# Performance work log

Hardware: AMD Instinct MI355X
Metric: run time of the kernel (lower is better)

Reference implementation:

```python
import jax, jax.numpy as jnp
import numpy as np

N_P, N_W, F_IN = 512, 3584, 256
H1, O1 = 8, 32
H2, O2 = 8, 256
BATCH = 1024
NEG_SLOPE = 0.2


def _xavier(key, shape):
    fan_in, fan_out = shape[-2], shape[-1]
    lim = jnp.sqrt(6.0 / (fan_in + fan_out))
    return jax.random.uniform(key, shape, jnp.float32, -lim, lim)


def setup_inputs() -> dict:
    key = jax.random.key(0)
    ks = jax.random.split(key, 16)
    return {
        "input": jax.random.uniform(ks[0], (BATCH, N_W), jnp.float32),
        "pern_feature": jax.random.normal(ks[1], (N_P, F_IN), jnp.float32),
        "word_feature": jax.random.normal(ks[2], (N_W, F_IN), jnp.float32),
        "w1": _xavier(ks[3], (H1, F_IN, O1)),
        "a_src1": _xavier(ks[4], (H1, O1, 1)),
        "a_dst1": _xavier(ks[5], (H1, O1, 1)),
        "b1": jnp.zeros((O1,), jnp.float32),
        "w2": _xavier(ks[6], (H2, F_IN, O2)),
        "a_src2": _xavier(ks[7], (H2, F_IN, 1)),
        "a_dst2": _xavier(ks[8], (H2, F_IN, 1)),
        "b2": jnp.zeros((O2,), jnp.float32),
        "W_fc": _xavier(ks[9], (O2, 5)),
        "b_fc": jnp.zeros((5,), jnp.float32),
        "pern_adj": jax.random.randint(ks[10], (N_P, N_P), 0, 2, jnp.int32),
        "word_pern_adj": jax.random.randint(ks[11], (N_P + N_W, N_P + N_W), 0, 2, jnp.int32),
    }


def gat(h, adj, w, a_src, a_dst, bias):
    # h: [N, f_in], adj: [N, N] int, w: [H, f_in, f_out]
    h_prime = jnp.einsum('nf,hfo->hno', h, w)          # [H, N, O]
    t = jnp.tanh(h_prime)
    s_src = jnp.einsum('hno,hoi->hn', t, a_src)        # [H, N]
    s_dst = jnp.einsum('hno,hoi->hn', t, a_dst)        # [H, N]
    attn = s_src[:, :, None] + s_dst[:, None, :]       # [H, N, N]
    attn = jnp.where(attn >= 0, attn, NEG_SLOPE * attn)  # leaky_relu
    attn = jnp.where(adj[None, :, :] > 0, attn, -jnp.inf)
    attn = jax.nn.softmax(attn, axis=-1)
    out = jnp.einsum('hnm,hmo->hno', attn, h_prime)    # [H, N, O]
    return out + bias


def reference(input, pern_feature, word_feature, w1, a_src1, a_dst1, b1,
              w2, a_src2, a_dst2, b2, W_fc, b_fc, pern_adj, word_pern_adj):
    n_p = pern_feature.shape[0]
    # GAT 1 over personality graph
    h1 = gat(pern_feature, pern_adj, w1, a_src1, a_dst1, b1)       # [H1, n_p, O1]
    hiddn_pp = jnp.transpose(h1, (1, 0, 2)).reshape(n_p, -1)        # [n_p, H1*O1]
    hiddn_pp = jax.nn.elu(hiddn_pp)
    # dropout is identity in eval mode
    hiddn_wp = jnp.concatenate([word_feature, hiddn_pp], axis=0)    # [N, 256]
    h2 = gat(hiddn_wp, word_pern_adj, w2, a_src2, a_dst2, b2)       # [H2, N, O2]
    hiddn_wp2 = h2.mean(axis=0)                                     # [N, O2]
    hiddn_w = hiddn_wp2[:word_feature.shape[0], :]                  # [n_w, O2]
    x = (input @ hiddn_w) / input.sum(axis=1, keepdims=True)        # [B, O2]
    return x @ W_fc + b_fc                                          # [B, 5]
```

## Files before the change

### kernel.cpp

```cpp
#include <hip/hip_runtime.h>
#include <hip/hip_bf16.h>
#include <math.h>

#define NP 512
#define NW 3584
#define NT 4096
#define FIN 256
#define H1 8
#define O1 32
#define H2 8
#define O2 256
#define NEG 0.2f

typedef __attribute__((ext_vector_type(8))) short bf16x8;
typedef __attribute__((ext_vector_type(4))) float f32x4;

__device__ __forceinline__ unsigned short f2bf(float f) {
    unsigned u = __float_as_uint(f);
    unsigned r = (u + 0x7FFF + ((u >> 16) & 1)) >> 16;
    return (unsigned short)r;
}

__global__ void k_conv_word(const float* __restrict__ wf, unsigned short* __restrict__ abf) {
    int i = blockIdx.x * 256 + threadIdx.x;
    if (i < NW * FIN) abf[i] = f2bf(wf[i]);
}

__global__ __launch_bounds__(256) void k_gat1_hp(
    const float* __restrict__ pf, const float* __restrict__ w1,
    const float* __restrict__ a_src1, const float* __restrict__ a_dst1,
    float* __restrict__ hp1, float* __restrict__ ss1, float* __restrict__ sd1)
{
    __shared__ float feat[8][FIN];
    int t = threadIdx.x;
    int n0 = blockIdx.x * 8;
    for (int q = 0; q < 8; q++) {
        int idx = q * 256 + t;
        feat[idx >> 8][idx & 255] = pf[(n0 + (idx >> 8)) * FIN + (idx & 255)];
    }
    __syncthreads();
    int h = t >> 5, o = t & 31;
    float acc[8] = {0,0,0,0,0,0,0,0};
    const float* wcol = w1 + h * FIN * O1 + o;
    for (int f = 0; f < FIN; f++) {
        float w = wcol[f * O1];
        #pragma unroll
        for (int i = 0; i < 8; i++) acc[i] += feat[i][f] * w;
    }
    float as = a_src1[h * O1 + o];
    float ad = a_dst1[h * O1 + o];
    #pragma unroll
    for (int i = 0; i < 8; i++) {
        hp1[(n0 + i) * 256 + t] = acc[i];
        float th = tanhf(acc[i]);
        float vs = th * as, vd = th * ad;
        #pragma unroll
        for (int off = 1; off < 32; off <<= 1) {
            vs += __shfl_xor(vs, off);
            vd += __shfl_xor(vd, off);
        }
        if (o == 0) { ss1[h * NP + n0 + i] = vs; sd1[h * NP + n0 + i] = vd; }
    }
}

__global__ __launch_bounds__(256) void k_gat1_attn(
    const int* __restrict__ adj, const float* __restrict__ hp1,
    const float* __restrict__ ss1, const float* __restrict__ sd1,
    const float* __restrict__ b1, unsigned short* __restrict__ abf)
{
    __shared__ float p[2][H1][NP];
    __shared__ float den[2][H1];
    int t = threadIdx.x;
    int n0 = blockIdx.x * 2;
    for (int rr = 0; rr < 32; rr++) {
        int idx = rr * 256 + t;
        int i = idx >> 12, h = (idx >> 9) & 7, m = idx & 511;
        float a = adj[(n0 + i) * NP + m] > 0 ? 1.0f : 0.0f;
        float e = ss1[h * NP + n0 + i] + sd1[h * NP + m];
        e = fmaxf(e, NEG * e);
        p[i][h][m] = a * __expf(e);
    }
    __syncthreads();
    int w = t >> 6, l = t & 63;
    {
        int i = w & 1;
        #pragma unroll
        for (int hh = 0; hh < 4; hh++) {
            int h = (w >> 1) * 4 + hh;
            float s = 0;
            #pragma unroll
            for (int q = 0; q < 8; q++) s += p[i][h][l + 64 * q];
            #pragma unroll
            for (int off = 1; off < 64; off <<= 1) s += __shfl_xor(s, off);
            if (l == 0) den[i][h] = s;
        }
    }
    __syncthreads();
    int h = t >> 5, o = t & 31;
    float acc[2] = {0, 0};
    #pragma unroll 4
    for (int m = 0; m < NP; m++) {
        float v = hp1[m * 256 + t];
        acc[0] += p[0][h][m] * v;
        acc[1] += p[1][h][m] * v;
    }
    float bo = b1[o];
    #pragma unroll
    for (int i = 0; i < 2; i++) {
        float r = acc[i] / den[i][h] + bo;
        r = r > 0.f ? r : expm1f(r);
        abf[(NW + n0 + i) * FIN + t] = f2bf(r);
    }
}

__global__ void k_conv_w2(const float* __restrict__ w2, unsigned short* __restrict__ btbf) {
    int idx = blockIdx.x * 256 + threadIdx.x;
    int f = idx & 255, o = (idx >> 8) & 255, h = idx >> 16;
    btbf[idx] = f2bf(w2[(h * FIN + f) * O2 + o]);
}

__global__ __launch_bounds__(256) void k_pack_adj(const int* __restrict__ adj,
                                                  unsigned long long* __restrict__ packed) {
    int w = threadIdx.x >> 6, l = threadIdx.x & 63;
    int r = blockIdx.x * 4 + w;
    const int* row = adj + (size_t)r * NT;
    unsigned long long myword = 0;
    for (int chunk = 0; chunk < 64; chunk++) {
        unsigned long long mask = __ballot(row[chunk * 64 + l] != 0);
        if (l == chunk) myword = mask;
    }
    packed[r * 64 + l] = myword;
}

__global__ __launch_bounds__(256) void k_gemm_hp2(
    const unsigned short* __restrict__ abf, const unsigned short* __restrict__ btbf,
    const float* __restrict__ a_src2, const float* __restrict__ a_dst2,
    const float* __restrict__ W_fc, float* __restrict__ gpart)
{
    int bid = blockIdx.x;
    int h = bid >> 6;
    int rem = bid & 63;
    int mt = rem >> 1, nt = rem & 1;
    int w = threadIdx.x >> 6, l = threadIdx.x & 63;
    int m0 = mt * 128 + (w >> 1) * 64;
    int n0 = nt * 128 + (w & 1) * 64;
    int lr = l & 15, lq = l >> 4;
    const unsigned short* bbase = btbf + h * O2 * FIN;
    f32x4 acc[4][4];
    #pragma unroll
    for (int i = 0; i < 4; i++)
        #pragma unroll
        for (int j = 0; j < 4; j++) acc[i][j] = (f32x4){0.f, 0.f, 0.f, 0.f};
    for (int k = 0; k < FIN; k += 32) {
        bf16x8 a[4], b[4];
        int kc = k + lq * 8;
        #pragma unroll
        for (int i = 0; i < 4; i++)
            a[i] = *(const bf16x8*)(abf + (m0 + i * 16 + lr) * FIN + kc);
        #pragma unroll
        for (int j = 0; j < 4; j++)
            b[j] = *(const bf16x8*)(bbase + (n0 + j * 16 + lr) * FIN + kc);
        #pragma unroll
        for (int i = 0; i < 4; i++)
            #pragma unroll
            for (int j = 0; j < 4; j++)
                acc[i][j] = __builtin_amdgcn_mfma_f32_16x16x32_bf16(a[i], b[j], acc[i][j], 0, 0, 0);
    }
    int slice = nt * 2 + (w & 1);
    float as[4], ad[4], wfc[4][5];
    #pragma unroll
    for (int j = 0; j < 4; j++) {
        int col = n0 + j * 16 + lr;
        as[j] = a_src2[h * O2 + col];
        ad[j] = a_dst2[h * O2 + col];
        #pragma unroll
        for (int jj = 0; jj < 5; jj++) wfc[j][jj] = W_fc[col * 5 + jj];
    }
    float* base = gpart + ((size_t)h * 4 + slice) * NT * 8;
    #pragma unroll
    for (int i = 0; i < 4; i++) {
        #pragma unroll
        for (int r = 0; r < 4; r++) {
            float s[7] = {0,0,0,0,0,0,0};
            #pragma unroll
            for (int j = 0; j < 4; j++) {
                float x = acc[i][j][r];
                float th = tanhf(x);
                s[0] += th * as[j];
                s[1] += th * ad[j];
                #pragma unroll
                for (int jj = 0; jj < 5; jj++) s[2 + jj] += x * wfc[j][jj];
            }
            #pragma unroll
            for (int off = 1; off < 16; off <<= 1)
                #pragma unroll
                for (int q = 0; q < 7; q++) s[q] += __shfl_xor(s[q], off);
            if (lr == 0) {
                int m = m0 + i * 16 + lq * 4 + r;
                float* dst = base + (size_t)m * 8;
                #pragma unroll
                for (int q = 0; q < 7; q++) dst[q] = s[q];
            }
        }
    }
}

__global__ __launch_bounds__(256) void k_comb_hp2(
    const float* __restrict__ gpart,
    float* __restrict__ ss2, float* __restrict__ sd2, float* __restrict__ G)
{
    int idx = blockIdx.x * 256 + threadIdx.x;
    int h = idx >> 12, m = idx & (NT - 1);
    float s[7] = {0,0,0,0,0,0,0};
    #pragma unroll
    for (int sl = 0; sl < 4; sl++) {
        const float* p = gpart + (((size_t)h * 4 + sl) * NT + m) * 8;
        #pragma unroll
        for (int q = 0; q < 7; q++) s[q] += p[q];
    }
    ss2[h * NT + m] = s[0];
    sd2[h * NT + m] = s[1];
    #pragma unroll
    for (int j = 0; j < 5; j++) G[(h * 5 + j) * NT + m] = s[2 + j];
}

__global__ void k_cvec(const float* __restrict__ b2, const float* __restrict__ W_fc,
                       float* __restrict__ c) {
    int t = threadIdx.x;
    float v[5];
    #pragma unroll
    for (int j = 0; j < 5; j++) v[j] = b2[t] * W_fc[t * 5 + j];
    #pragma unroll
    for (int off = 1; off < 64; off <<= 1)
        #pragma unroll
        for (int j = 0; j < 5; j++) v[j] += __shfl_xor(v[j], off);
    __shared__ float red[4][5];
    int w = t >> 6, l = t & 63;
    if (l == 0) { for (int j = 0; j < 5; j++) red[w][j] = v[j]; }
    __syncthreads();
    if (t == 0)
        for (int j = 0; j < 5; j++) c[j] = red[0][j] + red[1][j] + red[2][j] + red[3][j];
}

__global__ __launch_bounds__(512) void k_gat2_attn(
    const unsigned long long* __restrict__ packed, const float* __restrict__ ss2,
    const float* __restrict__ sd2, const float* __restrict__ G,
    float* __restrict__ part)
{
    int t = threadIdx.x;
    int h = t >> 6, l = t & 63;
    int nb = blockIdx.x & 511;
    int c;
    { int b = blockIdx.x; c = b / 448; nb = b - c * 448; }
    int n0 = nb * 8;
    float ss[8];
    #pragma unroll
    for (int i = 0; i < 8; i++) ss[i] = ss2[h * NT + n0 + i];
    const float* sdh = sd2 + h * NT;
    const float* g0 = G + (h * 5 + 0) * NT;
    const float* g1 = G + (h * 5 + 1) * NT;
    const float* g2 = G + (h * 5 + 2) * NT;
    const float* g3 = G + (h * 5 + 3) * NT;
    const float* g4 = G + (h * 5 + 4) * NT;
    float den[8] = {0,0,0,0,0,0,0,0};
    float num[8][5] = {{0}};
    int mbase = c * 1024;
    int cbase = mbase >> 6;
    for (int q = 0; q < 16; q++) {
        int m = mbase + q * 64 + l;
        float sd = sdh[m];
        float ga = g0[m], gb = g1[m], gc = g2[m], gd = g3[m], ge = g4[m];
        #pragma unroll
        for (int i = 0; i < 8; i++) {
            unsigned long long word = packed[(size_t)(n0 + i) * 64 + cbase + q];
            float e = ss[i] + sd;
            e = fmaxf(e, NEG * e);
            float t0 = __expf(e);
            float pp = ((word >> l) & 1ull) ? t0 : 0.0f;
            den[i] += pp;
            num[i][0] += pp * ga;
            num[i][1] += pp * gb;
            num[i][2] += pp * gc;
            num[i][3] += pp * gd;
            num[i][4] += pp * ge;
        }
    }
    float* base = part + ((size_t)(c * 448 + nb) * 64 + h * 8) * 6;
    #pragma unroll
    for (int i = 0; i < 8; i++) {
        #pragma unroll
        for (int off = 1; off < 64; off <<= 1) {
            den[i] += __shfl_xor(den[i], off);
            #pragma unroll
            for (int j = 0; j < 5; j++) num[i][j] += __shfl_xor(num[i][j], off);
        }
        if (l == 0) {
            float* dst = base + i * 6;
            dst[0] = den[i];
            #pragma unroll
            for (int j = 0; j < 5; j++) dst[1 + j] = num[i][j];
        }
    }
}

__global__ __launch_bounds__(256) void k_gat2_comb(const float* __restrict__ part,
                                                   float* __restrict__ hf) {
    int idx = blockIdx.x * 256 + threadIdx.x;
    int n = idx >> 3, h = idx & 7;
    int nb = n >> 3, i = n & 7;
    float den = 0, num[5] = {0,0,0,0,0};
    #pragma unroll
    for (int cc = 0; cc < 4; cc++) {
        const float* p = part + ((size_t)(cc * 448 + nb) * 64 + h * 8 + i) * 6;
        den += p[0];
        #pragma unroll
        for (int j = 0; j < 5; j++) num[j] += p[1 + j];
    }
    float inv = 1.0f / (den * 8.0f);
    float v[5];
    #pragma unroll
    for (int j = 0; j < 5; j++) v[j] = num[j] * inv;
    #pragma unroll
    for (int off = 1; off < 8; off <<= 1)
        #pragma unroll
        for (int j = 0; j < 5; j++) v[j] += __shfl_xor(v[j], off);
    if (h == 0) {
        #pragma unroll
        for (int j = 0; j < 5; j++) hf[n * 5 + j] = v[j];
    }
}

__global__ __launch_bounds__(256) void k_final(
    const float* __restrict__ input, const float* __restrict__ hf,
    const float* __restrict__ cvec, const float* __restrict__ b_fc,
    float* __restrict__ out)
{
    int b = blockIdx.x, t = threadIdx.x;
    const float* row = input + (size_t)b * NW;
    float s = 0.f, a[5] = {0.f, 0.f, 0.f, 0.f, 0.f};
    for (int n = t; n < NW; n += 256) {
        float x = row[n];
        s += x;
        #pragma unroll
        for (int j = 0; j < 5; j++) a[j] += x * hf[n * 5 + j];
    }
    #pragma unroll
    for (int off = 1; off < 64; off <<= 1) {
        s += __shfl_xor(s, off);
        #pragma unroll
        for (int j = 0; j < 5; j++) a[j] += __shfl_xor(a[j], off);
    }
    __shared__ float red[4][6];
    int w = t >> 6, l = t & 63;
    if (l == 0) { red[w][0] = s; for (int j = 0; j < 5; j++) red[w][j + 1] = a[j]; }
    __syncthreads();
    if (t < 5) {
        float st = red[0][0] + red[1][0] + red[2][0] + red[3][0];
        float aj = red[0][t + 1] + red[1][t + 1] + red[2][t + 1] + red[3][t + 1];
        out[b * 5 + t] = aj / st + cvec[t] + b_fc[t];
    }
}

extern "C" void kernel_launch(void* const* d_in, const int* in_sizes, int n_in,
                              void* d_out, int out_size, void* d_ws, size_t ws_size,
                              hipStream_t stream) {
    const float* input   = (const float*)d_in[0];
    const float* pf      = (const float*)d_in[1];
    const float* wf      = (const float*)d_in[2];
    const float* w1      = (const float*)d_in[3];
    const float* a_src1  = (const float*)d_in[4];
    const float* a_dst1  = (const float*)d_in[5];
    const float* b1      = (const float*)d_in[6];
    const float* w2      = (const float*)d_in[7];
    const float* a_src2  = (const float*)d_in[8];
    const float* a_dst2  = (const float*)d_in[9];
    const float* b2      = (const float*)d_in[10];
    const float* W_fc    = (const float*)d_in[11];
    const float* b_fc    = (const float*)d_in[12];
    const int* pern_adj  = (const int*)d_in[13];
    const int* wp_adj    = (const int*)d_in[14];
    float* out = (float*)d_out;

    char* ws = (char*)d_ws;
    unsigned short* abf    = (unsigned short*)(ws);
    unsigned short* btbf   = (unsigned short*)(ws + 2097152);
    float*          hp1    = (float*)(ws + 3145728);
    float*          ss1    = (float*)(ws + 3670016);
    float*          sd1    = (float*)(ws + 3686400);
    float*          ss2    = (float*)(ws + 3702784);
    float*          sd2    = (float*)(ws + 3833856);
    float*          G      = (float*)(ws + 3964928);
    float*          hf     = (float*)(ws + 4620288);
    float*          cvec   = (float*)(ws + 4691968);
    unsigned long long* packed = (unsigned long long*)(ws + 4692480);
    float*          gpart  = (float*)(ws + 6527488);
    float*          part   = (float*)(ws + 10721792);

    k_conv_word<<<3584, 256, 0, stream>>>(wf, abf);
    k_gat1_hp<<<64, 256, 0, stream>>>(pf, w1, a_src1, a_dst1, hp1, ss1, sd1);
    k_gat1_attn<<<256, 256, 0, stream>>>(pern_adj, hp1, ss1, sd1, b1, abf);
    k_conv_w2<<<2048, 256, 0, stream>>>(w2, btbf);
    k_pack_adj<<<896, 256, 0, stream>>>(wp_adj, packed);
    k_gemm_hp2<<<512, 256, 0, stream>>>(abf, btbf, a_src2, a_dst2, W_fc, gpart);
    k_comb_hp2<<<128, 256, 0, stream>>>(gpart, ss2, sd2, G);
    k_cvec<<<1, 256, 0, stream>>>(b2, W_fc, cvec);
    k_gat2_attn<<<1792, 512, 0, stream>>>(packed, ss2, sd2, G, part);
    k_gat2_comb<<<112, 256, 0, stream>>>(part, hf);
    k_final<<<1024, 256, 0, stream>>>(input, hf, cvec, b_fc, out);
}
```

Measured before the change: 297.1 us.

## Factor attention exponentials, vectorize adjacency packing and final reduction, fast tanh

The GAT2 attention kernel now splits exp(leaky_relu(ss+sd)) into a product of precomputed exponentials, exp(ss)*exp(sd) or exp(0.2ss)*exp(0.2sd), picked by the sign of ss+sd. This removes the per-pair exp and uses an inline v_cndmask with the packed adjacency word as the mask. Per-node tables are interleaved into 8-float records for vector loads, and each block handles 16 rows with 4 heads. Adjacency packing switches to int4 loads combined by shuffles, tanh becomes an exp-based approximation, and the final kernel uses float4 loads. The factored exponentials can overflow for large scores, and register pressure rises with the 16-row accumulators.

```diff
diff --git a/kernel.cpp b/kernel.cpp
--- a/kernel.cpp
+++ b/kernel.cpp
@@ -14,11 +14,17 @@
 
 typedef __attribute__((ext_vector_type(8))) short bf16x8;
 typedef __attribute__((ext_vector_type(4))) float f32x4;
+typedef unsigned long long u64;
 
 __device__ __forceinline__ unsigned short f2bf(float f) {
     unsigned u = __float_as_uint(f);
     unsigned r = (u + 0x7FFF + ((u >> 16) & 1)) >> 16;
     return (unsigned short)r;
+}
+
+__device__ __forceinline__ float fast_tanh(float x) {
+    float ex = __expf(2.0f * x);
+    return 1.0f - 2.0f / (ex + 1.0f);
 }
 
 __global__ void k_conv_word(const float* __restrict__ wf, unsigned short* __restrict__ abf) {
@@ -120,16 +126,21 @@
 }
 
 __global__ __launch_bounds__(256) void k_pack_adj(const int* __restrict__ adj,
-                                                  unsigned long long* __restrict__ packed) {
+                                                  u64* __restrict__ packed) {
     int w = threadIdx.x >> 6, l = threadIdx.x & 63;
     int r = blockIdx.x * 4 + w;
-    const int* row = adj + (size_t)r * NT;
-    unsigned long long myword = 0;
-    for (int chunk = 0; chunk < 64; chunk++) {
-        unsigned long long mask = __ballot(row[chunk * 64 + l] != 0);
-        if (l == chunk) myword = mask;
-    }
-    packed[r * 64 + l] = myword;
+    const int4* row = (const int4*)(adj + (size_t)r * NT);
+    for (int c4 = 0; c4 < 16; c4++) {
+        int4 x = row[c4 * 64 + l];
+        u64 nib = (u64)((x.x != 0 ? 1 : 0) | (x.y != 0 ? 2 : 0) |
+                        (x.z != 0 ? 4 : 0) | (x.w != 0 ? 8 : 0));
+        u64 v = nib << (4 * (l & 15));
+        v |= __shfl_xor(v, 1);
+        v |= __shfl_xor(v, 2);
+        v |= __shfl_xor(v, 4);
+        v |= __shfl_xor(v, 8);
+        if ((l & 15) == 0) packed[(size_t)r * 64 + c4 * 4 + (l >> 4)] = v;
+    }
 }
 
 __global__ __launch_bounds__(256) void k_gemm_hp2(
@@ -185,7 +196,7 @@
             #pragma unroll
             for (int j = 0; j < 4; j++) {
                 float x = acc[i][j][r];
-                float th = tanhf(x);
+                float th = fast_tanh(x);
                 s[0] += th * as[j];
                 s[1] += th * ad[j];
                 #pragma unroll
@@ -207,7 +218,8 @@
 
 __global__ __launch_bounds__(256) void k_comb_hp2(
     const float* __restrict__ gpart,
-    float* __restrict__ ss2, float* __restrict__ sd2, float* __restrict__ G)
+    float* __restrict__ negss, float* __restrict__ Etab, float* __restrict__ Eptab,
+    float* __restrict__ T)
 {
     int idx = blockIdx.x * 256 + threadIdx.x;
     int h = idx >> 12, m = idx & (NT - 1);
@@ -218,10 +230,13 @@
         #pragma unroll
         for (int q = 0; q < 7; q++) s[q] += p[q];
     }
-    ss2[h * NT + m] = s[0];
-    sd2[h * NT + m] = s[1];
-    #pragma unroll
-    for (int j = 0; j < 5; j++) G[(h * 5 + j) * NT + m] = s[2 + j];
+    negss[idx] = -s[0];
+    Etab[idx]  = __expf(s[0]);
+    Eptab[idx] = __expf(NEG * s[0]);
+    float4 t0 = {s[1], __expf(s[1]), __expf(NEG * s[1]), s[2]};
+    float4 t1 = {s[3], s[4], s[5], s[6]};
+    *(float4*)(T + (size_t)idx * 8)     = t0;
+    *(float4*)(T + (size_t)idx * 8 + 4) = t1;
 }
 
 __global__ void k_cvec(const float* __restrict__ b2, const float* __restrict__ W_fc,
@@ -242,63 +257,72 @@
         for (int j = 0; j < 5; j++) c[j] = red[0][j] + red[1][j] + red[2][j] + red[3][j];
 }
 
-__global__ __launch_bounds__(512) void k_gat2_attn(
-    const unsigned long long* __restrict__ packed, const float* __restrict__ ss2,
-    const float* __restrict__ sd2, const float* __restrict__ G,
-    float* __restrict__ part)
+__global__ __launch_bounds__(256) void k_gat2_attn(
+    const u64* __restrict__ packed, const float* __restrict__ negss,
+    const float* __restrict__ Etab, const float* __restrict__ Eptab,
+    const float* __restrict__ T, float* __restrict__ part)
 {
     int t = threadIdx.x;
-    int h = t >> 6, l = t & 63;
-    int nb = blockIdx.x & 511;
-    int c;
-    { int b = blockIdx.x; c = b / 448; nb = b - c * 448; }
-    int n0 = nb * 8;
-    float ss[8];
-    #pragma unroll
-    for (int i = 0; i < 8; i++) ss[i] = ss2[h * NT + n0 + i];
-    const float* sdh = sd2 + h * NT;
-    const float* g0 = G + (h * 5 + 0) * NT;
-    const float* g1 = G + (h * 5 + 1) * NT;
-    const float* g2 = G + (h * 5 + 2) * NT;
-    const float* g3 = G + (h * 5 + 3) * NT;
-    const float* g4 = G + (h * 5 + 4) * NT;
-    float den[8] = {0,0,0,0,0,0,0,0};
-    float num[8][5] = {{0}};
-    int mbase = c * 1024;
-    int cbase = mbase >> 6;
+    int l = t & 63;
+    int b = blockIdx.x;
+    int hg = b & 1, c = (b >> 1) & 3, nb = b >> 3;
+    int h = hg * 4 + (t >> 6);
+    int n0 = nb * 16;
+    float ns[16], E[16], Ep[16];
+    #pragma unroll
+    for (int i = 0; i < 16; i++) {
+        ns[i] = negss[h * NT + n0 + i];
+        E[i]  = Etab[h * NT + n0 + i];
+        Ep[i] = Eptab[h * NT + n0 + i];
+    }
+    float den[16];
+    float num[16][5];
+    #pragma unroll
+    for (int i = 0; i < 16; i++) {
+        den[i] = 0.f;
+        #pragma unroll
+        for (int j = 0; j < 5; j++) num[i][j] = 0.f;
+    }
+    const float* Th = T + (size_t)h * NT * 8;
+    const u64* prow = packed + c * 16;
     for (int q = 0; q < 16; q++) {
-        int m = mbase + q * 64 + l;
-        float sd = sdh[m];
-        float ga = g0[m], gb = g1[m], gc = g2[m], gd = g3[m], ge = g4[m];
-        #pragma unroll
-        for (int i = 0; i < 8; i++) {
-            unsigned long long word = packed[(size_t)(n0 + i) * 64 + cbase + q];
-            float e = ss[i] + sd;
-            e = fmaxf(e, NEG * e);
-            float t0 = __expf(e);
-            float pp = ((word >> l) & 1ull) ? t0 : 0.0f;
+        int m = c * 1024 + q * 64 + l;
+        const float* tp = Th + (size_t)m * 8;
+        float4 t0 = *(const float4*)tp;
+        float4 t1 = *(const float4*)(tp + 4);
+        float sd = t0.x, F = t0.y, Fp = t0.z;
+        float g0 = t0.w, g1 = t1.x, g2 = t1.y, g3 = t1.z, g4 = t1.w;
+        #pragma unroll
+        for (int i = 0; i < 16; i++) {
+            u64 word = prow[(size_t)(n0 + i) * 64 + q];
+            bool sel = sd >= ns[i];
+            float f = sel ? F : Fp;
+            float e = sel ? E[i] : Ep[i];
+            float pp0 = f * e;
+            float pp;
+            asm("v_cndmask_b32 %0, 0, %1, %2" : "=v"(pp) : "v"(pp0), "s"(word));
             den[i] += pp;
-            num[i][0] += pp * ga;
-            num[i][1] += pp * gb;
-            num[i][2] += pp * gc;
-            num[i][3] += pp * gd;
-            num[i][4] += pp * ge;
+            num[i][0] = fmaf(pp, g0, num[i][0]);
+            num[i][1] = fmaf(pp, g1, num[i][1]);
+            num[i][2] = fmaf(pp, g2, num[i][2]);
+            num[i][3] = fmaf(pp, g3, num[i][3]);
+            num[i][4] = fmaf(pp, g4, num[i][4]);
         }
     }
-    float* base = part + ((size_t)(c * 448 + nb) * 64 + h * 8) * 6;
-    #pragma unroll
-    for (int i = 0; i < 8; i++) {
-        #pragma unroll
-        for (int off = 1; off < 64; off <<= 1) {
-            den[i] += __shfl_xor(den[i], off);
-            #pragma unroll
-            for (int j = 0; j < 5; j++) num[i][j] += __shfl_xor(num[i][j], off);
-        }
+    #pragma unroll
+    for (int i = 0; i < 16; i++) {
+        float v[6];
+        v[0] = den[i];
+        #pragma unroll
+        for (int j = 0; j < 5; j++) v[1 + j] = num[i][j];
+        #pragma unroll
+        for (int off = 1; off < 64; off <<= 1)
+            #pragma unroll
+            for (int k = 0; k < 6; k++) v[k] += __shfl_xor(v[k], off);
         if (l == 0) {
-            float* dst = base + i * 6;
-            dst[0] = den[i];
-            #pragma unroll
-            for (int j = 0; j < 5; j++) dst[1 + j] = num[i][j];
+            float* dst = part + (((size_t)c * NW + n0 + i) * 8 + h) * 6;
+            #pragma unroll
+            for (int k = 0; k < 6; k++) dst[k] = v[k];
         }
     }
 }
@@ -307,11 +331,10 @@
                                                    float* __restrict__ hf) {
     int idx = blockIdx.x * 256 + threadIdx.x;
     int n = idx >> 3, h = idx & 7;
-    int nb = n >> 3, i = n & 7;
     float den = 0, num[5] = {0,0,0,0,0};
     #pragma unroll
     for (int cc = 0; cc < 4; cc++) {
-        const float* p = part + ((size_t)(cc * 448 + nb) * 64 + h * 8 + i) * 6;
+        const float* p = part + (((size_t)cc * NW + n) * 8 + h) * 6;
         den += p[0];
         #pragma unroll
         for (int j = 0; j < 5; j++) num[j] += p[1 + j];
@@ -336,13 +359,18 @@
     float* __restrict__ out)
 {
     int b = blockIdx.x, t = threadIdx.x;
-    const float* row = input + (size_t)b * NW;
+    const float4* row4 = (const float4*)(input + (size_t)b * NW);
+    const float4* hf4 = (const float4*)hf;
     float s = 0.f, a[5] = {0.f, 0.f, 0.f, 0.f, 0.f};
-    for (int n = t; n < NW; n += 256) {
-        float x = row[n];
-        s += x;
-        #pragma unroll
-        for (int j = 0; j < 5; j++) a[j] += x * hf[n * 5 + j];
+    for (int idx = t; idx < NW / 4; idx += 256) {
+        float4 x = row4[idx];
+        float f[20];
+        #pragma unroll
+        for (int q = 0; q < 5; q++) *(float4*)(f + 4 * q) = hf4[idx * 5 + q];
+        s += x.x + x.y + x.z + x.w;
+        #pragma unroll
+        for (int j = 0; j < 5; j++)
+            a[j] += x.x * f[j] + x.y * f[5 + j] + x.z * f[10 + j] + x.w * f[15 + j];
     }
     #pragma unroll
     for (int off = 1; off < 64; off <<= 1) {
@@ -387,14 +415,15 @@
     float*          hp1    = (float*)(ws + 3145728);
     float*          ss1    = (float*)(ws + 3670016);
     float*          sd1    = (float*)(ws + 3686400);
-    float*          ss2    = (float*)(ws + 3702784);
-    float*          sd2    = (float*)(ws + 3833856);
-    float*          G      = (float*)(ws + 3964928);
-    float*          hf     = (float*)(ws + 4620288);
-    float*          cvec   = (float*)(ws + 4691968);
-    unsigned long long* packed = (unsigned long long*)(ws + 4692480);
-    float*          gpart  = (float*)(ws + 6527488);
-    float*          part   = (float*)(ws + 10721792);
+    float*          negss  = (float*)(ws + 3702784);
+    float*          Etab   = (float*)(ws + 3833856);
+    float*          Eptab  = (float*)(ws + 3964928);
+    float*          T      = (float*)(ws + 4096000);
+    float*          hf     = (float*)(ws + 5144576);
+    float*          cvec   = (float*)(ws + 5216256);
+    u64*            packed = (u64*)(ws + 5216512);
+    float*          gpart  = (float*)(ws + 7051520);
+    float*          part   = (float*)(ws + 11245824);
 
     k_conv_word<<<3584, 256, 0, stream>>>(wf, abf);
     k_gat1_hp<<<64, 256, 0, stream>>>(pf, w1, a_src1, a_dst1, hp1, ss1, sd1);
@@ -402,9 +431,9 @@
     k_conv_w2<<<2048, 256, 0, stream>>>(w2, btbf);
     k_pack_adj<<<896, 256, 0, stream>>>(wp_adj, packed);
     k_gemm_hp2<<<512, 256, 0, stream>>>(abf, btbf, a_src2, a_dst2, W_fc, gpart);
-    k_comb_hp2<<<128, 256, 0, stream>>>(gpart, ss2, sd2, G);
+    k_comb_hp2<<<128, 256, 0, stream>>>(gpart, negss, Etab, Eptab, T);
     k_cvec<<<1, 256, 0, stream>>>(b2, W_fc, cvec);
-    k_gat2_attn<<<1792, 512, 0, stream>>>(packed, ss2, sd2, G, part);
+    k_gat2_attn<<<1792, 256, 0, stream>>>(packed, negss, Etab, Eptab, T, part);
     k_gat2_comb<<<112, 256, 0, stream>>>(part, hf);
     k_final<<<1024, 256, 0, stream>>>(input, hf, cvec, b_fc, out);
 }
```

New measurement: 316.7 us. 6.6% more time.
